# Kernel tuning notes

Hardware: AMD Instinct MI355X
Metric: run time of the kernel (lower is better)

The kernel has to match this reference:

```python
import jax, jax.numpy as jnp
import numpy as np
import math

D = 1024      # d_model
H = 16        # n_heads
DH = 64       # d_head
V = 32000     # vocab_size
MAXS = 2048   # max_seq_length
B, S = 2, 2048
PAD = 0
NEG = -1000000000.0
EPS = 1e-5


def _layernorm(x, g, b):
    mu = jnp.mean(x, axis=-1, keepdims=True)
    var = jnp.mean(jnp.square(x - mu), axis=-1, keepdims=True)
    return (x - mu) * jax.lax.rsqrt(var + EPS) * g + b


def _pad_mask(ids):
    # (b,1,1,S) additive mask over key columns where token == PAD
    return jnp.where((ids == PAD)[:, None, None, :], NEG, 0.0).astype(jnp.float32)


def _attn(Q, K, V_, out_w, out_b, causal_mask, pad_mask):
    # Q,K,V_: [b,n,s,d]
    logits = jnp.einsum('bnqd,bnkd->bnqk', Q, K) / math.sqrt(DH)
    if causal_mask is not None:
        logits = logits + causal_mask
    if pad_mask is not None:
        logits = logits + pad_mask
    probs = jax.nn.softmax(logits, axis=-1)
    o = jnp.einsum('bnqk,bnkd->bnqd', probs, V_)
    b, n, s, d = o.shape
    o = o.transpose(0, 2, 1, 3).reshape(b, s, n * d)  # b s (n d)
    return o @ out_w + out_b


def _heads(x, w, b):
    y = x @ w + b  # [b,s,H*DH]
    bs, s, _ = y.shape
    return y.reshape(bs, s, H, DH).transpose(0, 2, 1, 3)  # b n s d


def setup_inputs() -> dict:
    key = jax.random.key(0)
    ks = jax.random.split(key, 32)
    p = lambda i, shp, sc=0.02: (jax.random.normal(ks[i], shp, jnp.float32) * sc)
    inp = {
        'input_embedding': jax.random.normal(ks[0], (B, S, D), jnp.float32),
        'input_ids': jax.random.randint(ks[1], (B, S), 0, V),
        'target_ids': jax.random.randint(ks[2], (B, S), 0, V),
        'tok_emb': p(3, (V, D), 1.0),
        'pos_emb': p(4, (MAXS, D), 1.0),
        'ln1_g': jnp.ones((D,)), 'ln1_b': jnp.zeros((D,)),
        'q1_w': p(5, (D, H * DH)), 'q1_b': jnp.zeros((H * DH,)),
        'k1_w': p(6, (D, H * DH)), 'k1_b': jnp.zeros((H * DH,)),
        'v1_w': p(7, (D, H * DH)), 'v1_b': jnp.zeros((H * DH,)),
        'out1_w': p(8, (H * DH, D)), 'out1_b': jnp.zeros((D,)),
        'ln2_g': jnp.ones((D,)), 'ln2_b': jnp.zeros((D,)),
        'q2_w': p(9, (D, H * DH)), 'q2_b': jnp.zeros((H * DH,)),
        'k2_w': p(10, (D, H * DH)), 'k2_b': jnp.zeros((H * DH,)),
        'v2_w': p(11, (D, H * DH)), 'v2_b': jnp.zeros((H * DH,)),
        'out2_w': p(12, (H * DH, D)), 'out2_b': jnp.zeros((D,)),
        'ln3_g': jnp.ones((D,)), 'ln3_b': jnp.zeros((D,)),
        'mlp_w1': p(13, (D, 4 * D)), 'mlp_b1': jnp.zeros((4 * D,)),
        'mlp_w2': p(14, (4 * D, D)), 'mlp_b2': jnp.zeros((D,)),
    }
    return inp


def reference(input_embedding, input_ids, target_ids, tok_emb, pos_emb,
              ln1_g, ln1_b, q1_w, q1_b, k1_w, k1_b, v1_w, v1_b, out1_w, out1_b,
              ln2_g, ln2_b, q2_w, q2_b, k2_w, k2_b, v2_w, v2_b, out2_w, out2_b,
              ln3_g, ln3_b, mlp_w1, mlp_b1, mlp_w2, mlp_b2):
    b, s = target_ids.shape
    # embedding + positional
    x = tok_emb[target_ids] + pos_emb[jnp.arange(s)][None, :, :]
    x = _layernorm(x, ln1_g, ln1_b)
    # masked self-attention
    Q = _heads(x, q1_w, q1_b)
    K = _heads(x, k1_w, k1_b)
    Vv = _heads(x, v1_w, v1_b)
    causal = jnp.triu(jnp.full((s, s), NEG, jnp.float32), k=1)[None, None]
    attn = _attn(Q, K, Vv, out1_w, out1_b, causal, _pad_mask(target_ids))
    h = x + attn
    h = _layernorm(h, ln2_g, ln2_b)
    # cross-attention against encoder states
    Qc = _heads(h, q2_w, q2_b)
    Kc = _heads(input_embedding, k2_w, k2_b)
    Vc = _heads(input_embedding, v2_w, v2_b)
    cross = _attn(Qc, Kc, Vc, out2_w, out2_b, None, _pad_mask(input_ids))
    r = cross + h
    # MLP with exact GELU (torch nn.GELU default)
    z = _layernorm(r, ln3_g, ln3_b)
    mlp = jax.nn.gelu(z @ mlp_w1 + mlp_b1, approximate=False) @ mlp_w2 + mlp_b2
    return mlp + r
```

## Files before the change

### kernel.cpp

```cpp
#include <hip/hip_runtime.h>
#include <hip/hip_bf16.h>

#define S_LEN 2048
#define NEGF -1000000000.0f
#define QSC 0.18033688f

typedef unsigned short ushort_t;
typedef __attribute__((ext_vector_type(8))) short short8;
typedef __attribute__((ext_vector_type(4))) float f32x4;

#if defined(__has_builtin)
#if __has_builtin(__builtin_amdgcn_exp2f)
#define EXP2 __builtin_amdgcn_exp2f
#endif
#endif
#ifndef EXP2
#define EXP2 exp2f
#endif

__device__ __forceinline__ unsigned short f2b(float f) {
  unsigned int u = __float_as_uint(f);
  return (unsigned short)((u + 0x7fffu + ((u >> 16) & 1u)) >> 16);
}

__device__ __forceinline__ void gld_lds16(const void* g, void* l) {
  __builtin_amdgcn_global_load_lds((__attribute__((address_space(1))) unsigned int*)g,
                                   (__attribute__((address_space(3))) unsigned int*)l, 16, 0, 0);
}

__device__ __forceinline__ void wtrans_body(const float* __restrict__ W,
                                            ushort_t* __restrict__ Wt, int K, int N,
                                            int bx, int by) {
  __shared__ float t[32][33];
  int n0 = bx * 32, k0 = by * 32;
  int tx = threadIdx.x & 31, ty = threadIdx.x >> 5;
#pragma unroll
  for (int i = 0; i < 32; i += 8)
    t[ty + i][tx] = W[(size_t)(k0 + ty + i) * N + n0 + tx];
  __syncthreads();
#pragma unroll
  for (int i = 0; i < 32; i += 8)
    Wt[(size_t)(n0 + ty + i) * K + k0 + tx] = f2b(t[tx][ty + i]);
}

__global__ __launch_bounds__(256) void wtrans(const float* __restrict__ W,
                                              ushort_t* __restrict__ Wt, int K, int N) {
  wtrans_body(W, Wt, K, N, blockIdx.x, blockIdx.y);
}

struct P8 {
  const float* s[8];
  ushort_t* d[8];
};
__global__ __launch_bounds__(256) void wtrans8(P8 p) {
  wtrans_body(p.s[blockIdx.z], p.d[blockIdx.z], 1024, 1024, blockIdx.x, blockIdx.y);
}

__global__ __launch_bounds__(256) void f2bcvt(const float* __restrict__ in,
                                              ushort_t* __restrict__ out) {
  size_t i = ((size_t)blockIdx.x * 256 + threadIdx.x) * 4;
  float4 v = *(const float4*)(in + i);
  union { unsigned short u[4]; uint2 q; } pk;
  pk.u[0] = f2b(v.x); pk.u[1] = f2b(v.y); pk.u[2] = f2b(v.z); pk.u[3] = f2b(v.w);
  *(uint2*)(out + i) = pk.q;
}

__global__ __launch_bounds__(256) void bcat(float* __restrict__ dst, const float* __restrict__ a,
                                            const float* __restrict__ b,
                                            const float* __restrict__ c, int n0, int n1) {
  int i = blockIdx.x * 256 + threadIdx.x;
  float v = (i < n0) ? a[i] : (i < n0 + n1 ? b[i - n0] : c[i - n0 - n1]);
  dst[i] = v;
}

__device__ __forceinline__ void row_stats(float s, float ss, float* outMean, float* outRstd) {
  __shared__ float red[8];
#pragma unroll
  for (int o = 32; o > 0; o >>= 1) {
    s += __shfl_down(s, o);
    ss += __shfl_down(ss, o);
  }
  int wave = threadIdx.x >> 6, lane = threadIdx.x & 63;
  if (lane == 0) { red[wave] = s; red[4 + wave] = ss; }
  __syncthreads();
  if (threadIdx.x == 0) {
    float S0 = red[0] + red[1] + red[2] + red[3];
    float S1 = red[4] + red[5] + red[6] + red[7];
    float mean = S0 * (1.0f / 1024.0f);
    float var = S1 * (1.0f / 1024.0f) - mean * mean;
    red[0] = mean;
    red[1] = rsqrtf(var + 1e-5f);
  }
  __syncthreads();
  *outMean = red[0];
  *outRstd = red[1];
}

__global__ __launch_bounds__(256) void embed_ln(const int* __restrict__ tids,
                                                const float* __restrict__ tok,
                                                const float* __restrict__ pos,
                                                const float* __restrict__ g,
                                                const float* __restrict__ be,
                                                float* __restrict__ xf,
                                                ushort_t* __restrict__ xb) {
  int row = blockIdx.x;
  int s = row & (S_LEN - 1);
  int id = tids[row];
  int c = threadIdx.x * 4;
  float4 v = *(const float4*)(tok + (size_t)id * 1024 + c);
  float4 p = *(const float4*)(pos + (size_t)s * 1024 + c);
  v.x += p.x; v.y += p.y; v.z += p.z; v.w += p.w;
  float mean, rstd;
  row_stats(v.x + v.y + v.z + v.w, v.x * v.x + v.y * v.y + v.z * v.z + v.w * v.w, &mean, &rstd);
  float4 gv = *(const float4*)(g + c);
  float4 bv = *(const float4*)(be + c);
  float4 o;
  o.x = (v.x - mean) * rstd * gv.x + bv.x;
  o.y = (v.y - mean) * rstd * gv.y + bv.y;
  o.z = (v.z - mean) * rstd * gv.z + bv.z;
  o.w = (v.w - mean) * rstd * gv.w + bv.w;
  *(float4*)(xf + (size_t)row * 1024 + c) = o;
  union { unsigned short u[4]; uint2 q; } pk;
  pk.u[0] = f2b(o.x); pk.u[1] = f2b(o.y); pk.u[2] = f2b(o.z); pk.u[3] = f2b(o.w);
  *(uint2*)(xb + (size_t)row * 1024 + c) = pk.q;
}

__global__ __launch_bounds__(256) void ln_fwd(const float* in, const float* __restrict__ g,
                                              const float* __restrict__ be, float* outF,
                                              ushort_t* __restrict__ outB) {
  int row = blockIdx.x;
  int c = threadIdx.x * 4;
  float4 v = *(const float4*)(in + (size_t)row * 1024 + c);
  float mean, rstd;
  row_stats(v.x + v.y + v.z + v.w, v.x * v.x + v.y * v.y + v.z * v.z + v.w * v.w, &mean, &rstd);
  float4 gv = *(const float4*)(g + c);
  float4 bv = *(const float4*)(be + c);
  float4 o;
  o.x = (v.x - mean) * rstd * gv.x + bv.x;
  o.y = (v.y - mean) * rstd * gv.y + bv.y;
  o.z = (v.z - mean) * rstd * gv.z + bv.z;
  o.w = (v.w - mean) * rstd * gv.w + bv.w;
  if (outF) *(float4*)(outF + (size_t)row * 1024 + c) = o;
  union { unsigned short u[4]; uint2 q; } pk;
  pk.u[0] = f2b(o.x); pk.u[1] = f2b(o.y); pk.u[2] = f2b(o.z); pk.u[3] = f2b(o.w);
  *(uint2*)(outB + (size_t)row * 1024 + c) = pk.q;
}

__global__ __launch_bounds__(256) void gemm_bt(const ushort_t* __restrict__ A,
                                               const ushort_t* __restrict__ Bt,
                                               const float* __restrict__ bias,
                                               const float* __restrict__ res,
                                               float* __restrict__ outF,
                                               ushort_t* __restrict__ outB,
                                               ushort_t* __restrict__ outT,
                                               int M, int N, int K, int act, int scaleN,
                                               int nSplit) {
  __shared__ __align__(16) ushort_t lA[128 * 64];
  __shared__ __align__(16) ushort_t lB[128 * 64];
  const int tid = threadIdx.x;
  const int wave = tid >> 6, lane = tid & 63;
  const int quad = lane >> 4, l16 = lane & 15;
  const int m0 = blockIdx.y * 128, n0 = blockIdx.x * 128;
  const int wm = (wave >> 1) * 64, wn = (wave & 1) * 64;

  f32x4 zero4 = {0.f, 0.f, 0.f, 0.f};
  f32x4 acc[4][4];
#pragma unroll
  for (int i = 0; i < 4; ++i)
#pragma unroll
    for (int j = 0; j < 4; ++j) acc[i][j] = zero4;

  int rowS[4], chkS[4];
#pragma unroll
  for (int ii = 0; ii < 4; ++ii) {
    int d = (wave * 4 + ii) * 64 + lane;
    rowS[ii] = d >> 3;
    chkS[ii] = (d & 7) ^ (rowS[ii] & 7);
  }

  for (int kt = 0; kt < K; kt += 64) {
    __syncthreads();
#pragma unroll
    for (int ii = 0; ii < 4; ++ii) {
      gld_lds16(A + (size_t)(m0 + rowS[ii]) * K + kt + chkS[ii] * 8,
                (char*)lA + (wave * 4 + ii) * 1024);
      gld_lds16(Bt + (size_t)(n0 + rowS[ii]) * K + kt + chkS[ii] * 8,
                (char*)lB + (wave * 4 + ii) * 1024);
    }
    __syncthreads();
#pragma unroll
    for (int kc = 0; kc < 2; ++kc) {
      short8 af[4], bf[4];
#pragma unroll
      for (int mt = 0; mt < 4; ++mt) {
        int r = wm + mt * 16 + l16;
        int c = (kc * 4 + quad) ^ (r & 7);
        af[mt] = *(const short8*)(lA + r * 64 + c * 8);
      }
#pragma unroll
      for (int nt = 0; nt < 4; ++nt) {
        int r = wn + nt * 16 + l16;
        int c = (kc * 4 + quad) ^ (r & 7);
        bf[nt] = *(const short8*)(lB + r * 64 + c * 8);
      }
#pragma unroll
      for (int mt = 0; mt < 4; ++mt)
#pragma unroll
        for (int nt = 0; nt < 4; ++nt)
          acc[mt][nt] = __builtin_amdgcn_mfma_f32_16x16x32_bf16(af[mt], bf[nt], acc[mt][nt], 0, 0, 0);
    }
  }

#pragma unroll
  for (int nt = 0; nt < 4; ++nt) {
    int gn = n0 + wn + nt * 16 + l16;
    float bv = bias[gn];
    if (gn < nSplit) {
#pragma unroll
      for (int mt = 0; mt < 4; ++mt) {
        int gmb = m0 + wm + mt * 16 + quad * 4;
#pragma unroll
        for (int reg = 0; reg < 4; ++reg) {
          size_t idx = (size_t)(gmb + reg) * nSplit + gn;
          float v = acc[mt][nt][reg] + bv;
          if (act == 1) v = 0.5f * v * (1.0f + erff(v * 0.70710678118654752f));
          if (gn < scaleN) v *= QSC;
          if (res) v += res[idx];
          if (outF) outF[idx] = v;
          if (outB) outB[idx] = f2b(v);
        }
      }
    } else {
#pragma unroll
      for (int mt = 0; mt < 4; ++mt) {
        int gmb = m0 + wm + mt * 16 + quad * 4;
        union { unsigned short u[4]; uint2 q; } pk;
#pragma unroll
        for (int reg = 0; reg < 4; ++reg) pk.u[reg] = f2b(acc[mt][nt][reg] + bv);
        *(uint2*)(outT + (size_t)(gn - nSplit) * M + gmb) = pk.q;
      }
    }
  }
}

__global__ __launch_bounds__(256) void gemm_n64(const ushort_t* __restrict__ A,
                                                const ushort_t* __restrict__ Bt,
                                                const float* __restrict__ bias,
                                                const float* __restrict__ res,
                                                float* __restrict__ outF,
                                                ushort_t* __restrict__ outB,
                                                int M, int N, int K, int act, int scaleN) {
  __shared__ __align__(16) ushort_t lA[128 * 64];
  __shared__ __align__(16) ushort_t lB[64 * 64];
  const int tid = threadIdx.x;
  const int wave = tid >> 6, lane = tid & 63;
  const int quad = lane >> 4, l16 = lane & 15;
  const int m0 = blockIdx.y * 128, n0 = blockIdx.x * 64;
  const int wm = wave * 32;

  f32x4 zero4 = {0.f, 0.f, 0.f, 0.f};
  f32x4 acc[2][4];
#pragma unroll
  for (int i = 0; i < 2; ++i)
#pragma unroll
    for (int j = 0; j < 4; ++j) acc[i][j] = zero4;

  int rowA[4], chkA[4], rowB[2], chkB[2];
#pragma unroll
  for (int ii = 0; ii < 4; ++ii) {
    int d = (wave * 4 + ii) * 64 + lane;
    rowA[ii] = d >> 3;
    chkA[ii] = (d & 7) ^ (rowA[ii] & 7);
  }
#pragma unroll
  for (int ii = 0; ii < 2; ++ii) {
    int d = (wave * 2 + ii) * 64 + lane;
    rowB[ii] = d >> 3;
    chkB[ii] = (d & 7) ^ (rowB[ii] & 7);
  }

  for (int kt = 0; kt < K; kt += 64) {
    __syncthreads();
#pragma unroll
    for (int ii = 0; ii < 4; ++ii)
      gld_lds16(A + (size_t)(m0 + rowA[ii]) * K + kt + chkA[ii] * 8,
                (char*)lA + (wave * 4 + ii) * 1024);
#pragma unroll
    for (int ii = 0; ii < 2; ++ii)
      gld_lds16(Bt + (size_t)(n0 + rowB[ii]) * K + kt + chkB[ii] * 8,
                (char*)lB + (wave * 2 + ii) * 1024);
    __syncthreads();
#pragma unroll
    for (int kc = 0; kc < 2; ++kc) {
      short8 af[2], bf[4];
#pragma unroll
      for (int mt = 0; mt < 2; ++mt) {
        int r = wm + mt * 16 + l16;
        int c = (kc * 4 + quad) ^ (r & 7);
        af[mt] = *(const short8*)(lA + r * 64 + c * 8);
      }
#pragma unroll
      for (int nt = 0; nt < 4; ++nt) {
        int r = nt * 16 + l16;
        int c = (kc * 4 + quad) ^ (r & 7);
        bf[nt] = *(const short8*)(lB + r * 64 + c * 8);
      }
#pragma unroll
      for (int mt = 0; mt < 2; ++mt)
#pragma unroll
        for (int nt = 0; nt < 4; ++nt)
          acc[mt][nt] = __builtin_amdgcn_mfma_f32_16x16x32_bf16(af[mt], bf[nt], acc[mt][nt], 0, 0, 0);
    }
  }

#pragma unroll
  for (int nt = 0; nt < 4; ++nt) {
    int gn = n0 + nt * 16 + l16;
    float bv = bias[gn];
#pragma unroll
    for (int mt = 0; mt < 2; ++mt) {
      int gmb = m0 + wm + mt * 16 + quad * 4;
#pragma unroll
      for (int reg = 0; reg < 4; ++reg) {
        size_t idx = (size_t)(gmb + reg) * N + gn;
        float v = acc[mt][nt][reg] + bv;
        if (act == 1) v = 0.5f * v * (1.0f + erff(v * 0.70710678118654752f));
        if (gn < scaleN) v *= QSC;
        if (res) v += res[idx];
        if (outF) outF[idx] = v;
        if (outB) outB[idx] = f2b(v);
      }
    }
  }
}

template <int CAUSAL>
__global__ __launch_bounds__(256, 4) void attn3(const ushort_t* __restrict__ Qp, int ldQ,
                                                const ushort_t* __restrict__ Kp, int ldK,
                                                const ushort_t* __restrict__ Vt,
                                                const int* __restrict__ ids,
                                                ushort_t* __restrict__ O) {
  __shared__ float pm[S_LEN];
  __shared__ __align__(16) ushort_t lK[64 * 64];
  __shared__ __align__(16) ushort_t lVt[64 * 64];
  __shared__ __align__(16) ushort_t lP[4][16 * 64];

  const int h = blockIdx.y, b = blockIdx.z;
  const int g = CAUSAL ? (31 - (int)blockIdx.x) : (int)blockIdx.x;
  const int tid = threadIdx.x;
  const int wave = tid >> 6, lane = tid & 63;
  const int quad = lane >> 4, l16 = lane & 15;
  const int g0 = g * 64;

  for (int i = tid; i < S_LEN; i += 256)
    pm[i] = (ids[b * S_LEN + i] == 0) ? NEGF : 0.0f;

  const int qrow = g0 + wave * 16 + l16;
  const ushort_t* qb = Qp + ((size_t)(b * S_LEN) + qrow) * ldQ + h * 64;
  short8 qf[2];
  qf[0] = *(const short8*)(qb + quad * 8);
  qf[1] = *(const short8*)(qb + 32 + quad * 8);

  f32x4 zero4 = {0.f, 0.f, 0.f, 0.f};
  f32x4 acc_o[4];
#pragma unroll
  for (int nt = 0; nt < 4; ++nt) acc_o[nt] = zero4;
  float lsum[4] = {0.f, 0.f, 0.f, 0.f};

  const int nkv = CAUSAL ? (g + 1) : (S_LEN / 64);
  const int qbase = g0 + wave * 16 + quad * 4;

  for (int kv = 0; kv < nkv; ++kv) {
    const int kv0 = kv * 64;
    __syncthreads();
#pragma unroll
    for (int ii = 0; ii < 2; ++ii) {
      int slot = (wave * 2 + ii) * 64 + lane;
      int row = slot >> 3;
      int cs = (slot & 7) ^ (row & 7);
      gld_lds16(Kp + (size_t)(b * S_LEN + kv0 + row) * ldK + h * 64 + cs * 8,
                (char*)lK + (wave * 2 + ii) * 1024);
      gld_lds16(Vt + (size_t)(h * 64 + row) * 4096 + b * S_LEN + kv0 + cs * 8,
                (char*)lVt + (wave * 2 + ii) * 1024);
    }
    __syncthreads();

    f32x4 sacc[4];
#pragma unroll
    for (int nt = 0; nt < 4; ++nt) sacc[nt] = zero4;
#pragma unroll
    for (int kc = 0; kc < 2; ++kc) {
#pragma unroll
      for (int nt = 0; nt < 4; ++nt) {
        int r = nt * 16 + l16;
        int c = (kc * 4 + quad) ^ (r & 7);
        short8 kf = *(const short8*)(lK + r * 64 + c * 8);
        sacc[nt] = __builtin_amdgcn_mfma_f32_16x16x32_bf16(qf[kc], kf, sacc[nt], 0, 0, 0);
      }
    }

    const bool diag = CAUSAL && (kv == g);
#pragma unroll
    for (int nt = 0; nt < 4; ++nt) {
      float pmv = pm[kv0 + nt * 16 + l16];
      int kk = kv0 + nt * 16 + l16;
#pragma unroll
      for (int reg = 0; reg < 4; ++reg) {
        float s = sacc[nt][reg] + pmv;
        if (diag && kk > qbase + reg) s = NEGF;
        float p = EXP2(s);
        lsum[reg] += p;
        int q = quad * 4 + reg;
        int cc = (nt * 2 + (l16 >> 3)) ^ (q & 7);
        lP[wave][q * 64 + cc * 8 + (l16 & 7)] = f2b(p);
      }
    }

#pragma unroll
    for (int kc = 0; kc < 2; ++kc) {
      int cp = (kc * 4 + quad) ^ (l16 & 7);
      short8 pf = *(const short8*)(&lP[wave][l16 * 64 + cp * 8]);
#pragma unroll
      for (int nt = 0; nt < 4; ++nt) {
        int r = nt * 16 + l16;
        int c = (kc * 4 + quad) ^ (r & 7);
        short8 vf = *(const short8*)(lVt + r * 64 + c * 8);
        acc_o[nt] = __builtin_amdgcn_mfma_f32_16x16x32_bf16(pf, vf, acc_o[nt], 0, 0, 0);
      }
    }
  }

  float inv[4];
#pragma unroll
  for (int reg = 0; reg < 4; ++reg) {
    float t = lsum[reg];
    t += __shfl_xor(t, 1);
    t += __shfl_xor(t, 2);
    t += __shfl_xor(t, 4);
    t += __shfl_xor(t, 8);
    inv[reg] = 1.0f / t;
  }
#pragma unroll
  for (int nt = 0; nt < 4; ++nt)
#pragma unroll
    for (int reg = 0; reg < 4; ++reg) {
      int qr = g0 + wave * 16 + quad * 4 + reg;
      O[((size_t)(b * S_LEN) + qr) * 1024 + h * 64 + nt * 16 + l16] =
          f2b(acc_o[nt][reg] * inv[reg]);
    }
}

extern "C" void kernel_launch(void* const* d_in, const int* in_sizes, int n_in,
                              void* d_out, int out_size, void* d_ws, size_t ws_size,
                              hipStream_t stream) {
  (void)in_sizes; (void)n_in; (void)out_size; (void)ws_size;
  const size_t MB = 1024 * 1024;
  char* w = (char*)d_ws;
  ushort_t* qkv1T = (ushort_t*)(w + 0);
  ushort_t* o1T = (ushort_t*)(w + 6 * MB);
  ushort_t* q2T = (ushort_t*)(w + 8 * MB);
  ushort_t* k2v2T = (ushort_t*)(w + 10 * MB);
  ushort_t* o2T = (ushort_t*)(w + 14 * MB);
  ushort_t* m1T = (ushort_t*)(w + 16 * MB);
  ushort_t* m2T = (ushort_t*)(w + 24 * MB);
  float* bias3 = (float*)(w + 32 * MB);
  float* bias2 = (float*)(w + 32 * MB + 64 * 1024);
  ushort_t* xb = (ushort_t*)(w + 33 * MB);
  ushort_t* QKb = (ushort_t*)(w + 41 * MB);
  ushort_t* Vt = (ushort_t*)(w + 57 * MB);
  ushort_t* Ob = (ushort_t*)(w + 65 * MB);
  ushort_t* encb = (ushort_t*)(w + 73 * MB);
  float* xf = (float*)(w + 81 * MB);
  float* hf = (float*)(w + 97 * MB);
  ushort_t* m1b = (ushort_t*)(w + 113 * MB);
  ushort_t* hlnb = xb;
  ushort_t* Q2b = QKb;
  ushort_t* K2b = QKb + 4 * MB;

  dim3 B256(256);
  P8 p8;
  p8.s[0] = (const float*)d_in[7];  p8.d[0] = qkv1T;
  p8.s[1] = (const float*)d_in[9];  p8.d[1] = qkv1T + 1024 * 1024;
  p8.s[2] = (const float*)d_in[11]; p8.d[2] = qkv1T + 2 * 1024 * 1024;
  p8.s[3] = (const float*)d_in[13]; p8.d[3] = o1T;
  p8.s[4] = (const float*)d_in[17]; p8.d[4] = q2T;
  p8.s[5] = (const float*)d_in[19]; p8.d[5] = k2v2T;
  p8.s[6] = (const float*)d_in[21]; p8.d[6] = k2v2T + 1024 * 1024;
  p8.s[7] = (const float*)d_in[23]; p8.d[7] = o2T;
  wtrans8<<<dim3(32, 32, 8), B256, 0, stream>>>(p8);
  wtrans<<<dim3(128, 32), B256, 0, stream>>>((const float*)d_in[27], m1T, 1024, 4096);
  wtrans<<<dim3(32, 128), B256, 0, stream>>>((const float*)d_in[29], m2T, 4096, 1024);
  f2bcvt<<<4096, B256, 0, stream>>>((const float*)d_in[0], encb);
  bcat<<<12, B256, 0, stream>>>(bias3, (const float*)d_in[8], (const float*)d_in[10],
                                (const float*)d_in[12], 1024, 1024);
  bcat<<<8, B256, 0, stream>>>(bias2, (const float*)d_in[20], (const float*)d_in[22],
                               (const float*)d_in[22], 1024, 1024);

  embed_ln<<<4096, B256, 0, stream>>>((const int*)d_in[2], (const float*)d_in[3],
                                      (const float*)d_in[4], (const float*)d_in[5],
                                      (const float*)d_in[6], xf, xb);
  gemm_bt<<<dim3(24, 32), B256, 0, stream>>>(xb, qkv1T, bias3, nullptr, nullptr, QKb, Vt,
                                             4096, 3072, 1024, 0, 1024, 2048);
  attn3<1><<<dim3(32, 16, 2), B256, 0, stream>>>(QKb, 2048, QKb + 1024, 2048, Vt,
                                                 (const int*)d_in[2], Ob);
  gemm_n64<<<dim3(16, 32), B256, 0, stream>>>(Ob, o1T, (const float*)d_in[14], xf, hf, nullptr,
                                              4096, 1024, 1024, 0, 0);
  ln_fwd<<<4096, B256, 0, stream>>>(hf, (const float*)d_in[15], (const float*)d_in[16], hf, hlnb);
  gemm_n64<<<dim3(16, 32), B256, 0, stream>>>(hlnb, q2T, (const float*)d_in[18], nullptr, nullptr,
                                              Q2b, 4096, 1024, 1024, 0, 1024);
  gemm_bt<<<dim3(16, 32), B256, 0, stream>>>(encb, k2v2T, bias2, nullptr, nullptr, K2b, Vt,
                                             4096, 2048, 1024, 0, 0, 1024);
  attn3<0><<<dim3(32, 16, 2), B256, 0, stream>>>(Q2b, 1024, K2b, 1024, Vt,
                                                 (const int*)d_in[1], Ob);
  gemm_n64<<<dim3(16, 32), B256, 0, stream>>>(Ob, o2T, (const float*)d_in[24], hf, xf, nullptr,
                                              4096, 1024, 1024, 0, 0);
  ln_fwd<<<4096, B256, 0, stream>>>(xf, (const float*)d_in[25], (const float*)d_in[26], nullptr,
                                    hlnb);
  gemm_bt<<<dim3(32, 32), B256, 0, stream>>>(hlnb, m1T, (const float*)d_in[28], nullptr, nullptr,
                                             m1b, nullptr, 4096, 4096, 1024, 1, 0, 4096);
  gemm_n64<<<dim3(16, 32), B256, 0, stream>>>(m1b, m2T, (const float*)d_in[30], xf, (float*)d_out,
                                              nullptr, 4096, 1024, 4096, 0, 0);
}
```

Baseline: 693.2 us.

## Add 256x256-tile double-buffered MFMA GEMM for QKV, cross-KV and MLP1

```diff
diff --git a/kernel.cpp b/kernel.cpp
--- a/kernel.cpp
+++ b/kernel.cpp
@@ -243,6 +243,137 @@
   }
 }
 
+__global__ __launch_bounds__(512, 2) void gemm256(const ushort_t* __restrict__ A,
+                                                  const ushort_t* __restrict__ Bt,
+                                                  const float* __restrict__ bias,
+                                                  const float* __restrict__ res,
+                                                  float* __restrict__ outF,
+                                                  ushort_t* __restrict__ outB,
+                                                  ushort_t* __restrict__ outT,
+                                                  int M, int N, int K, int act, int scaleN,
+                                                  int nSplit) {
+  __shared__ __align__(16) ushort_t sA[2][256 * 64];
+  __shared__ __align__(16) ushort_t sB[2][256 * 64];
+  const int tid = threadIdx.x;
+  const int wave = tid >> 6, lane = tid & 63;
+  const int quad = lane >> 4, l16 = lane & 15;
+  const int m0 = blockIdx.y * 256, n0 = blockIdx.x * 256;
+  const int wm = (wave >> 2) * 128, wn = (wave & 3) * 64;
+
+  const ushort_t* Ab = A + (size_t)m0 * K;
+  const ushort_t* Bb = Bt + (size_t)n0 * K;
+
+  const int srow = tid >> 3;
+  const int schk = ((tid & 7) ^ (srow & 7)) << 3;
+
+#define STAGE_H(SRC, LD, KT, DST, H)                                          \
+  do {                                                                        \
+    gld_lds16((SRC) + (size_t)((H) * 128 + srow) * (LD) + (KT) + schk,        \
+              (char*)(DST) + (H) * 16384 + tid * 16);                         \
+    gld_lds16((SRC) + (size_t)((H) * 128 + 64 + srow) * (LD) + (KT) + schk,   \
+              (char*)(DST) + (H) * 16384 + 8192 + tid * 16);                  \
+  } while (0)
+
+  f32x4 zero4 = {0.f, 0.f, 0.f, 0.f};
+  f32x4 acc[8][4];
+#pragma unroll
+  for (int i = 0; i < 8; ++i)
+#pragma unroll
+    for (int j = 0; j < 4; ++j) acc[i][j] = zero4;
+
+  const int NT = K >> 6;
+
+  STAGE_H(Ab, K, 0, sA[0], 0);
+  STAGE_H(Ab, K, 0, sA[0], 1);
+  STAGE_H(Bb, K, 0, sB[0], 0);
+  STAGE_H(Bb, K, 0, sB[0], 1);
+  asm volatile("s_waitcnt vmcnt(0)" ::: "memory");
+  __builtin_amdgcn_s_barrier();
+
+  for (int t = 0; t < NT; ++t) {
+    const ushort_t* curA = sA[t & 1];
+    const ushort_t* curB = sB[t & 1];
+    ushort_t* nxtA = sA[(t + 1) & 1];
+    ushort_t* nxtB = sB[(t + 1) & 1];
+    const int ktn = (t + 1) << 6;
+    const bool more = (t + 1 < NT);
+#pragma unroll
+    for (int q = 0; q < 4; ++q) {
+      const int mh = q >> 1, nh = q & 1;
+      short8 af[4][2], bf[2][2];
+#pragma unroll
+      for (int mt = 0; mt < 4; ++mt)
+#pragma unroll
+        for (int kc = 0; kc < 2; ++kc) {
+          int r = wm + (mh * 4 + mt) * 16 + l16;
+          af[mt][kc] = *(const short8*)(curA + r * 64 + (((kc * 4 + quad) ^ (r & 7)) << 3));
+        }
+#pragma unroll
+      for (int nt = 0; nt < 2; ++nt)
+#pragma unroll
+        for (int kc = 0; kc < 2; ++kc) {
+          int r = wn + (nh * 2 + nt) * 16 + l16;
+          bf[nt][kc] = *(const short8*)(curB + r * 64 + (((kc * 4 + quad) ^ (r & 7)) << 3));
+        }
+      if (more) {
+        if (q == 0) {
+          STAGE_H(Ab, K, ktn, nxtA, 0);
+          STAGE_H(Ab, K, ktn, nxtA, 1);
+        } else if (q == 1) {
+          STAGE_H(Bb, K, ktn, nxtB, 0);
+          STAGE_H(Bb, K, ktn, nxtB, 1);
+        }
+      }
+      __builtin_amdgcn_s_barrier();
+      asm volatile("s_waitcnt lgkmcnt(0)" ::: "memory");
+      __builtin_amdgcn_s_setprio(1);
+#pragma unroll
+      for (int mt = 0; mt < 4; ++mt)
+#pragma unroll
+        for (int nt = 0; nt < 2; ++nt)
+#pragma unroll
+          for (int kc = 0; kc < 2; ++kc)
+            acc[mh * 4 + mt][nh * 2 + nt] = __builtin_amdgcn_mfma_f32_16x16x32_bf16(
+                af[mt][kc], bf[nt][kc], acc[mh * 4 + mt][nh * 2 + nt], 0, 0, 0);
+      __builtin_amdgcn_s_setprio(0);
+      if (q == 3) asm volatile("s_waitcnt vmcnt(0)" ::: "memory");
+      __builtin_amdgcn_s_barrier();
+    }
+  }
+#undef STAGE_H
+
+#pragma unroll
+  for (int nt = 0; nt < 4; ++nt) {
+    int gn = n0 + wn + nt * 16 + l16;
+    float bv = bias[gn];
+    if (gn < nSplit) {
+#pragma unroll
+      for (int mt = 0; mt < 8; ++mt) {
+        int gmb = m0 + wm + mt * 16 + quad * 4;
+#pragma unroll
+        for (int reg = 0; reg < 4; ++reg) {
+          size_t idx = (size_t)(gmb + reg) * nSplit + gn;
+          float v = acc[mt][nt][reg] + bv;
+          if (act == 1) v = 0.5f * v * (1.0f + erff(v * 0.70710678118654752f));
+          if (gn < scaleN) v *= QSC;
+          if (res) v += res[idx];
+          if (outF) outF[idx] = v;
+          if (outB) outB[idx] = f2b(v);
+        }
+      }
+    } else {
+#pragma unroll
+      for (int mt = 0; mt < 8; ++mt) {
+        int gmb = m0 + wm + mt * 16 + quad * 4;
+        union { unsigned short u[4]; uint2 q2; } pk;
+#pragma unroll
+        for (int reg = 0; reg < 4; ++reg) pk.u[reg] = f2b(acc[mt][nt][reg] + bv);
+        *(uint2*)(outT + (size_t)(gn - nSplit) * M + gmb) = pk.q2;
+      }
+    }
+  }
+}
+
 __global__ __launch_bounds__(256) void gemm_n64(const ushort_t* __restrict__ A,
                                                 const ushort_t* __restrict__ Bt,
                                                 const float* __restrict__ bias,
@@ -478,6 +609,7 @@
   ushort_t* K2b = QKb + 4 * MB;
 
   dim3 B256(256);
+  dim3 B512(512);
   P8 p8;
   p8.s[0] = (const float*)d_in[7];  p8.d[0] = qkv1T;
   p8.s[1] = (const float*)d_in[9];  p8.d[1] = qkv1T + 1024 * 1024;
@@ -499,7 +631,7 @@
   embed_ln<<<4096, B256, 0, stream>>>((const int*)d_in[2], (const float*)d_in[3],
                                       (const float*)d_in[4], (const float*)d_in[5],
                                       (const float*)d_in[6], xf, xb);
-  gemm_bt<<<dim3(24, 32), B256, 0, stream>>>(xb, qkv1T, bias3, nullptr, nullptr, QKb, Vt,
+  gemm256<<<dim3(12, 16), B512, 0, stream>>>(xb, qkv1T, bias3, nullptr, nullptr, QKb, Vt,
                                              4096, 3072, 1024, 0, 1024, 2048);
   attn3<1><<<dim3(32, 16, 2), B256, 0, stream>>>(QKb, 2048, QKb + 1024, 2048, Vt,
                                                  (const int*)d_in[2], Ob);
@@ -508,15 +640,15 @@
   ln_fwd<<<4096, B256, 0, stream>>>(hf, (const float*)d_in[15], (const float*)d_in[16], hf, hlnb);
   gemm_n64<<<dim3(16, 32), B256, 0, stream>>>(hlnb, q2T, (const float*)d_in[18], nullptr, nullptr,
                                               Q2b, 4096, 1024, 1024, 0, 1024);
-  gemm_bt<<<dim3(16, 32), B256, 0, stream>>>(encb, k2v2T, bias2, nullptr, nullptr, K2b, Vt,
-                                             4096, 2048, 1024, 0, 0, 1024);
+  gemm256<<<dim3(8, 16), B512, 0, stream>>>(encb, k2v2T, bias2, nullptr, nullptr, K2b, Vt,
+                                            4096, 2048, 1024, 0, 0, 1024);
   attn3<0><<<dim3(32, 16, 2), B256, 0, stream>>>(Q2b, 1024, K2b, 1024, Vt,
                                                  (const int*)d_in[1], Ob);
   gemm_n64<<<dim3(16, 32), B256, 0, stream>>>(Ob, o2T, (const float*)d_in[24], hf, xf, nullptr,
                                               4096, 1024, 1024, 0, 0);
   ln_fwd<<<4096, B256, 0, stream>>>(xf, (const float*)d_in[25], (const float*)d_in[26], nullptr,
                                     hlnb);
-  gemm_bt<<<dim3(32, 32), B256, 0, stream>>>(hlnb, m1T, (const float*)d_in[28], nullptr, nullptr,
+  gemm256<<<dim3(16, 16), B512, 0, stream>>>(hlnb, m1T, (const float*)d_in[28], nullptr, nullptr,
                                              m1b, nullptr, 4096, 4096, 1024, 1, 0, 4096);
   gemm_n64<<<dim3(16, 32), B256, 0, stream>>>(m1b, m2T, (const float*)d_in[30], xf, (float*)d_out,
                                               nullptr, 4096, 1024, 4096, 0, 0);
```

New measurement: 748.5 us. 8.0% more time.

## Process two query tiles per attention block with double-buffered K/V staging

Applied to the files above, without the earlier changes.

```diff
diff --git a/kernel.cpp b/kernel.cpp
--- a/kernel.cpp
+++ b/kernel.cpp
@@ -71,6 +71,15 @@
   int i = blockIdx.x * 256 + threadIdx.x;
   float v = (i < n0) ? a[i] : (i < n0 + n1 ? b[i - n0] : c[i - n0 - n1]);
   dst[i] = v;
+}
+
+__global__ __launch_bounds__(256) void padmask(const int* __restrict__ tids,
+                                               const int* __restrict__ iids,
+                                               float* __restrict__ pmA,
+                                               float* __restrict__ pmB) {
+  int i = blockIdx.x * 256 + threadIdx.x;
+  pmA[i] = (tids[i] == 0) ? NEGF : 0.0f;
+  pmB[i] = (iids[i] == 0) ? NEGF : 0.0f;
 }
 
 __device__ __forceinline__ void row_stats(float s, float ss, float* outMean, float* outRstd) {
@@ -335,119 +344,154 @@
 }
 
 template <int CAUSAL>
-__global__ __launch_bounds__(256, 4) void attn3(const ushort_t* __restrict__ Qp, int ldQ,
+__global__ __launch_bounds__(256, 2) void attn6(const ushort_t* __restrict__ Qp, int ldQ,
                                                 const ushort_t* __restrict__ Kp, int ldK,
                                                 const ushort_t* __restrict__ Vt,
-                                                const int* __restrict__ ids,
+                                                const float* __restrict__ pmg,
                                                 ushort_t* __restrict__ O) {
-  __shared__ float pm[S_LEN];
-  __shared__ __align__(16) ushort_t lK[64 * 64];
-  __shared__ __align__(16) ushort_t lVt[64 * 64];
+  __shared__ __align__(16) ushort_t lK[2][64 * 64];
+  __shared__ __align__(16) ushort_t lV[2][64 * 64];
   __shared__ __align__(16) ushort_t lP[4][16 * 64];
 
   const int h = blockIdx.y, b = blockIdx.z;
-  const int g = CAUSAL ? (31 - (int)blockIdx.x) : (int)blockIdx.x;
+  const int bx = blockIdx.x;
+  const int gq[2] = {CAUSAL ? (31 - bx) : (2 * bx), CAUSAL ? bx : (2 * bx + 1)};
   const int tid = threadIdx.x;
   const int wave = tid >> 6, lane = tid & 63;
   const int quad = lane >> 4, l16 = lane & 15;
-  const int g0 = g * 64;
-
-  for (int i = tid; i < S_LEN; i += 256)
-    pm[i] = (ids[b * S_LEN + i] == 0) ? NEGF : 0.0f;
-
-  const int qrow = g0 + wave * 16 + l16;
-  const ushort_t* qb = Qp + ((size_t)(b * S_LEN) + qrow) * ldQ + h * 64;
-  short8 qf[2];
-  qf[0] = *(const short8*)(qb + quad * 8);
-  qf[1] = *(const short8*)(qb + 32 + quad * 8);
+  const float* pmb = pmg + b * S_LEN;
+
+  short8 qf[2][2];
+#pragma unroll
+  for (int s = 0; s < 2; ++s) {
+    const ushort_t* qb =
+        Qp + ((size_t)(b * S_LEN) + gq[s] * 64 + wave * 16 + l16) * ldQ + h * 64;
+    qf[s][0] = *(const short8*)(qb + quad * 8);
+    qf[s][1] = *(const short8*)(qb + 32 + quad * 8);
+  }
 
   f32x4 zero4 = {0.f, 0.f, 0.f, 0.f};
-  f32x4 acc_o[4];
-#pragma unroll
-  for (int nt = 0; nt < 4; ++nt) acc_o[nt] = zero4;
-  float lsum[4] = {0.f, 0.f, 0.f, 0.f};
-
-  const int nkv = CAUSAL ? (g + 1) : (S_LEN / 64);
-  const int qbase = g0 + wave * 16 + quad * 4;
-
+  f32x4 acc_o[2][4];
+  float lsum[2][4];
+#pragma unroll
+  for (int s = 0; s < 2; ++s)
+#pragma unroll
+    for (int nt = 0; nt < 4; ++nt) {
+      acc_o[s][nt] = zero4;
+      lsum[s][nt] = 0.f;
+    }
+
+  const int nkv = CAUSAL ? (gq[0] + 1) : (S_LEN / 64);
+
+  int srow[2], scs[2];
+#pragma unroll
+  for (int ii = 0; ii < 2; ++ii) {
+    int slot = (wave * 2 + ii) * 64 + lane;
+    srow[ii] = slot >> 3;
+    scs[ii] = ((slot & 7) ^ (srow[ii] & 7)) * 8;
+  }
+
+#define STAGE_KV(KV0, BUF)                                                            \
+  do {                                                                                \
+    _Pragma("unroll") for (int ii = 0; ii < 2; ++ii) {                                \
+      gld_lds16(Kp + (size_t)(b * S_LEN + (KV0) + srow[ii]) * ldK + h * 64 + scs[ii], \
+                (char*)lK[BUF] + (wave * 2 + ii) * 1024);                             \
+      gld_lds16(Vt + (size_t)(h * 64 + srow[ii]) * 4096 + b * S_LEN + (KV0) + scs[ii],\
+                (char*)lV[BUF] + (wave * 2 + ii) * 1024);                             \
+    }                                                                                 \
+  } while (0)
+
+  STAGE_KV(0, 0);
+  __syncthreads();
+
+  int cur = 0;
   for (int kv = 0; kv < nkv; ++kv) {
     const int kv0 = kv * 64;
-    __syncthreads();
-#pragma unroll
-    for (int ii = 0; ii < 2; ++ii) {
-      int slot = (wave * 2 + ii) * 64 + lane;
-      int row = slot >> 3;
-      int cs = (slot & 7) ^ (row & 7);
-      gld_lds16(Kp + (size_t)(b * S_LEN + kv0 + row) * ldK + h * 64 + cs * 8,
-                (char*)lK + (wave * 2 + ii) * 1024);
-      gld_lds16(Vt + (size_t)(h * 64 + row) * 4096 + b * S_LEN + kv0 + cs * 8,
-                (char*)lVt + (wave * 2 + ii) * 1024);
-    }
-    __syncthreads();
-
-    f32x4 sacc[4];
-#pragma unroll
-    for (int nt = 0; nt < 4; ++nt) sacc[nt] = zero4;
-#pragma unroll
-    for (int kc = 0; kc < 2; ++kc) {
+    if (kv + 1 < nkv) STAGE_KV(kv0 + 64, cur ^ 1);
+
+    float pmv[4];
+#pragma unroll
+    for (int nt = 0; nt < 4; ++nt) pmv[nt] = pmb[kv0 + nt * 16 + l16];
+
+    const ushort_t* cK = lK[cur];
+    const ushort_t* cV = lV[cur];
+
+    short8 kf[2][4], vf[2][4];
+#pragma unroll
+    for (int kc = 0; kc < 2; ++kc)
 #pragma unroll
       for (int nt = 0; nt < 4; ++nt) {
         int r = nt * 16 + l16;
         int c = (kc * 4 + quad) ^ (r & 7);
-        short8 kf = *(const short8*)(lK + r * 64 + c * 8);
-        sacc[nt] = __builtin_amdgcn_mfma_f32_16x16x32_bf16(qf[kc], kf, sacc[nt], 0, 0, 0);
-      }
-    }
-
-    const bool diag = CAUSAL && (kv == g);
-#pragma unroll
-    for (int nt = 0; nt < 4; ++nt) {
-      float pmv = pm[kv0 + nt * 16 + l16];
-      int kk = kv0 + nt * 16 + l16;
+        kf[kc][nt] = *(const short8*)(cK + r * 64 + c * 8);
+        vf[kc][nt] = *(const short8*)(cV + r * 64 + c * 8);
+      }
+
+#pragma unroll
+    for (int s = 0; s < 2; ++s) {
+      if (CAUSAL && kv > gq[s]) continue;
+
+      f32x4 sacc[4];
+#pragma unroll
+      for (int nt = 0; nt < 4; ++nt) sacc[nt] = zero4;
+#pragma unroll
+      for (int kc = 0; kc < 2; ++kc)
+#pragma unroll
+        for (int nt = 0; nt < 4; ++nt)
+          sacc[nt] = __builtin_amdgcn_mfma_f32_16x16x32_bf16(qf[s][kc], kf[kc][nt], sacc[nt], 0, 0, 0);
+
+      const int qbase = gq[s] * 64 + wave * 16 + quad * 4;
+      const bool diag = CAUSAL && (kv == gq[s]);
+#pragma unroll
+      for (int nt = 0; nt < 4; ++nt) {
+        int kk = kv0 + nt * 16 + l16;
+#pragma unroll
+        for (int reg = 0; reg < 4; ++reg) {
+          float sv = sacc[nt][reg] + pmv[nt];
+          if (diag && kk > qbase + reg) sv = NEGF;
+          float p = EXP2(sv);
+          lsum[s][reg] += p;
+          int q = quad * 4 + reg;
+          int cc = (nt * 2 + (l16 >> 3)) ^ (q & 7);
+          lP[wave][q * 64 + cc * 8 + (l16 & 7)] = f2b(p);
+        }
+      }
+
+#pragma unroll
+      for (int kc = 0; kc < 2; ++kc) {
+        int cp = (kc * 4 + quad) ^ (l16 & 7);
+        short8 pf = *(const short8*)(&lP[wave][l16 * 64 + cp * 8]);
+#pragma unroll
+        for (int nt = 0; nt < 4; ++nt)
+          acc_o[s][nt] = __builtin_amdgcn_mfma_f32_16x16x32_bf16(pf, vf[kc][nt], acc_o[s][nt], 0, 0, 0);
+      }
+    }
+    __syncthreads();
+    cur ^= 1;
+  }
+#undef STAGE_KV
+
+#pragma unroll
+  for (int s = 0; s < 2; ++s) {
+    float inv[4];
+#pragma unroll
+    for (int reg = 0; reg < 4; ++reg) {
+      float t = lsum[s][reg];
+      t += __shfl_xor(t, 1);
+      t += __shfl_xor(t, 2);
+      t += __shfl_xor(t, 4);
+      t += __shfl_xor(t, 8);
+      inv[reg] = 1.0f / t;
+    }
+#pragma unroll
+    for (int nt = 0; nt < 4; ++nt)
 #pragma unroll
       for (int reg = 0; reg < 4; ++reg) {
-        float s = sacc[nt][reg] + pmv;
-        if (diag && kk > qbase + reg) s = NEGF;
-        float p = EXP2(s);
-        lsum[reg] += p;
-        int q = quad * 4 + reg;
-        int cc = (nt * 2 + (l16 >> 3)) ^ (q & 7);
-        lP[wave][q * 64 + cc * 8 + (l16 & 7)] = f2b(p);
-      }
-    }
-
-#pragma unroll
-    for (int kc = 0; kc < 2; ++kc) {
-      int cp = (kc * 4 + quad) ^ (l16 & 7);
-      short8 pf = *(const short8*)(&lP[wave][l16 * 64 + cp * 8]);
-#pragma unroll
-      for (int nt = 0; nt < 4; ++nt) {
-        int r = nt * 16 + l16;
-        int c = (kc * 4 + quad) ^ (r & 7);
-        short8 vf = *(const short8*)(lVt + r * 64 + c * 8);
-        acc_o[nt] = __builtin_amdgcn_mfma_f32_16x16x32_bf16(pf, vf, acc_o[nt], 0, 0, 0);
-      }
-    }
-  }
-
-  float inv[4];
-#pragma unroll
-  for (int reg = 0; reg < 4; ++reg) {
-    float t = lsum[reg];
-    t += __shfl_xor(t, 1);
-    t += __shfl_xor(t, 2);
-    t += __shfl_xor(t, 4);
-    t += __shfl_xor(t, 8);
-    inv[reg] = 1.0f / t;
-  }
-#pragma unroll
-  for (int nt = 0; nt < 4; ++nt)
-#pragma unroll
-    for (int reg = 0; reg < 4; ++reg) {
-      int qr = g0 + wave * 16 + quad * 4 + reg;
-      O[((size_t)(b * S_LEN) + qr) * 1024 + h * 64 + nt * 16 + l16] =
-          f2b(acc_o[nt][reg] * inv[reg]);
-    }
+        int qr = gq[s] * 64 + wave * 16 + quad * 4 + reg;
+        O[((size_t)(b * S_LEN) + qr) * 1024 + h * 64 + nt * 16 + l16] =
+            f2b(acc_o[s][nt][reg] * inv[reg]);
+      }
+  }
 }
 
 extern "C" void kernel_launch(void* const* d_in, const int* in_sizes, int n_in,
@@ -465,6 +509,8 @@
   ushort_t* m2T = (ushort_t*)(w + 24 * MB);
   float* bias3 = (float*)(w + 32 * MB);
   float* bias2 = (float*)(w + 32 * MB + 64 * 1024);
+  float* pmA = (float*)(w + 32 * MB + 128 * 1024);
+  float* pmB = (float*)(w + 32 * MB + 160 * 1024);
   ushort_t* xb = (ushort_t*)(w + 33 * MB);
   ushort_t* QKb = (ushort_t*)(w + 41 * MB);
   ushort_t* Vt = (ushort_t*)(w + 57 * MB);
@@ -495,14 +541,14 @@
                                 (const float*)d_in[12], 1024, 1024);
   bcat<<<8, B256, 0, stream>>>(bias2, (const float*)d_in[20], (const float*)d_in[22],
                                (const float*)d_in[22], 1024, 1024);
+  padmask<<<16, B256, 0, stream>>>((const int*)d_in[2], (const int*)d_in[1], pmA, pmB);
 
   embed_ln<<<4096, B256, 0, stream>>>((const int*)d_in[2], (const float*)d_in[3],
                                       (const float*)d_in[4], (const float*)d_in[5],
                                       (const float*)d_in[6], xf, xb);
   gemm_bt<<<dim3(24, 32), B256, 0, stream>>>(xb, qkv1T, bias3, nullptr, nullptr, QKb, Vt,
                                              4096, 3072, 1024, 0, 1024, 2048);
-  attn3<1><<<dim3(32, 16, 2), B256, 0, stream>>>(QKb, 2048, QKb + 1024, 2048, Vt,
-                                                 (const int*)d_in[2], Ob);
+  attn6<1><<<dim3(16, 16, 2), B256, 0, stream>>>(QKb, 2048, QKb + 1024, 2048, Vt, pmA, Ob);
   gemm_n64<<<dim3(16, 32), B256, 0, stream>>>(Ob, o1T, (const float*)d_in[14], xf, hf, nullptr,
                                               4096, 1024, 1024, 0, 0);
   ln_fwd<<<4096, B256, 0, stream>>>(hf, (const float*)d_in[15], (const float*)d_in[16], hf, hlnb);
@@ -510,8 +556,7 @@
                                               Q2b, 4096, 1024, 1024, 0, 1024);
   gemm_bt<<<dim3(16, 32), B256, 0, stream>>>(encb, k2v2T, bias2, nullptr, nullptr, K2b, Vt,
                                              4096, 2048, 1024, 0, 0, 1024);
-  attn3<0><<<dim3(32, 16, 2), B256, 0, stream>>>(Q2b, 1024, K2b, 1024, Vt,
-                                                 (const int*)d_in[1], Ob);
+  attn6<0><<<dim3(16, 16, 2), B256, 0, stream>>>(Q2b, 1024, K2b, 1024, Vt, pmB, Ob);
   gemm_n64<<<dim3(16, 32), B256, 0, stream>>>(Ob, o2T, (const float*)d_in[24], hf, xf, nullptr,
                                               4096, 1024, 1024, 0, 0);
   ln_fwd<<<4096, B256, 0, stream>>>(xf, (const float*)d_in[25], (const float*)d_in[26], nullptr,
```

Measured after the change: 688.6 us. No clear change (-0.7%).
